# Optimization experiments

Hardware: AMD Instinct MI355X
Metric: run time of the kernel (lower is better)

The kernel has to match this reference:

```python
import jax, jax.numpy as jnp
import numpy as np

B, S, HQ, HKV, D = 2, 1024, 32, 8, 128

def setup_inputs() -> dict:
    key = jax.random.key(0)
    k1, k2, k3 = jax.random.split(key, 3)
    xq = jax.random.normal(k1, (B, S, HQ, D), dtype=jnp.float32)
    xk = jax.random.normal(k2, (B, S, HKV, D), dtype=jnp.float32)
    xv = jax.random.normal(k3, (B, S, HKV, D), dtype=jnp.float32)
    kv_buffer = jnp.zeros((B * S, 2 * HKV, D), dtype=jnp.float32)
    cur_select_index = jnp.arange(B * S, dtype=jnp.int64 if jax.config.read('jax_enable_x64') else jnp.int32)
    return {"xq": xq, "xk": xk, "xv": xv, "kv_buffer": kv_buffer,
            "cur_select_index": cur_select_index}


def reference(xq, xk, xv, kv_buffer, cur_select_index):
    b, s, hq, d = xq.shape
    hkv = xk.shape[2]
    group = hq // hkv

    # --- KV-cache scatter write: kv_buffer[cur_select_index] = cat(k, v) ---
    combined_kv = jnp.concatenate([xk, xv], axis=2).reshape(-1, 2 * hkv, d)
    kv_buffer_new = kv_buffer.at[cur_select_index].set(combined_kv)

    # --- causal flash-style prefill attention (GQA: repeat kv heads) ---
    scale = 1.0 / np.sqrt(d).astype(np.float32)
    k = jnp.repeat(xk, group, axis=2)  # [b, s, hq, d]
    v = jnp.repeat(xv, group, axis=2)

    scores = jnp.einsum('bqhd,bkhd->bhqk', xq, k) * scale  # [b, hq, s, s]
    causal = jnp.tril(jnp.ones((s, s), dtype=bool))
    scores = jnp.where(causal[None, None], scores, jnp.finfo(scores.dtype).min)
    attn = jax.nn.softmax(scores, axis=-1)
    out = jnp.einsum('bhqk,bkhd->bqhd', attn, v)  # [b, s, hq, d]
    out = out.reshape(b, s, hq * d)
    return out, kv_buffer_new
```

## Files before the change

kernel.cpp:

```cpp
#include <hip/hip_runtime.h>
#include <math.h>

#define B_  2
#define S_  1024
#define HQ_ 32
#define HKV_ 8
#define D_  128

typedef __bf16 bf16x8 __attribute__((ext_vector_type(8)));
typedef float  floatx4 __attribute__((ext_vector_type(4)));

static __device__ __forceinline__ unsigned pack2(float hi, float lo) {
    return __builtin_amdgcn_perm(__float_as_uint(hi), __float_as_uint(lo), 0x07060302u);
}

__global__ void kv_scatter_kernel(const float* __restrict__ xk,
                                  const float* __restrict__ xv,
                                  const int* __restrict__ sel,
                                  float* __restrict__ kv_out) {
    const int total = B_ * S_ * 2 * HKV_ * D_ / 4;
    for (int g = blockIdx.x * 256 + threadIdx.x; g < total; g += gridDim.x * 256) {
        const int t      = g >> 9;
        const int within = g & 511;
        const int idx    = sel[t];
        const float4* src = (within < 256)
            ? ((const float4*)(xk + (size_t)t * (HKV_ * D_)) + within)
            : ((const float4*)(xv + (size_t)t * (HKV_ * D_)) + (within - 256));
        ((float4*)(kv_out + (size_t)idx * (2 * HKV_ * D_)))[within] = *src;
    }
}

__global__ __launch_bounds__(256, 2)
void attn_kernel(const float* __restrict__ xq, const float* __restrict__ xk,
                 const float* __restrict__ xv, float* __restrict__ out) {
    const int lid = blockIdx.x;
    const int hk  = lid & 7;
    const int j   = lid >> 3;
    const int qq  = j & 31;
    const int b   = j >> 5;
    const int qt  = b ? (31 - qq) : qq;

    const int tid  = threadIdx.x;
    const int wave = tid >> 6;
    const int lane = tid & 63;
    const int l15  = lane & 15;
    const int quad = lane >> 4;
    const int L    = lane & 31;
    const int hi32 = lane >> 5;
    const int h    = hk * 4 + wave;

    __shared__ __align__(16) unsigned short Kl[2][32][136];
    __shared__ __align__(16) unsigned int   Vp[2][128][16];

    bf16x8 qf[2][4];
#pragma unroll
    for (int mt = 0; mt < 2; ++mt) {
        const int row = qt * 32 + mt * 16 + l15;
        const float* qp = xq + (((size_t)(b * S_ + row)) * HQ_ + h) * D_ + quad * 8;
#pragma unroll
        for (int ks = 0; ks < 4; ++ks) {
            union { bf16x8 v; unsigned u[4]; } t2;
            const float4 f0 = *(const float4*)(qp + ks * 32);
            const float4 f1 = *(const float4*)(qp + ks * 32 + 4);
            t2.u[0] = pack2(f0.y, f0.x); t2.u[1] = pack2(f0.w, f0.z);
            t2.u[2] = pack2(f1.y, f1.x); t2.u[3] = pack2(f1.w, f1.z);
            qf[mt][ks] = t2.v;
        }
    }

    bf16x8 ones;
    { union { bf16x8 v; unsigned u[4]; } o;
      o.u[0] = o.u[1] = o.u[2] = o.u[3] = 0x3F803F80u; ones = o.v; }

    floatx4 acc[2][8];
    floatx4 lacc[2];
#pragma unroll
    for (int mt = 0; mt < 2; ++mt) {
        lacc[mt] = (floatx4){0.f, 0.f, 0.f, 0.f};
#pragma unroll
        for (int n = 0; n < 8; ++n) acc[mt][n] = (floatx4){0.f, 0.f, 0.f, 0.f};
    }

    const float scale2 = 0.12751741f;

    float4 pk[4], pv[4];
    const int keyw = wave * 2 + hi32;

    auto loads = [&](int t) {
        const size_t base = ((size_t)(b * S_ + t * 32 + keyw) * HKV_ + hk) * D_ + 4 * L;
#pragma unroll
        for (int i = 0; i < 4; ++i) {
            pk[i] = *(const float4*)(xk + base + (size_t)i * 8 * HKV_ * D_);
            pv[i] = *(const float4*)(xv + base + (size_t)i * 8 * HKV_ * D_);
        }
    };

    auto writesLDS = [&](int bi) {
#pragma unroll
        for (int i = 0; i < 4; ++i) {
            const int key = i * 8 + keyw;
            unsigned kw0 = pack2(pk[i].y, pk[i].x), kw1 = pack2(pk[i].w, pk[i].z);
            *(uint2*)&Kl[bi][key][4 * L] = make_uint2(kw0, kw1);
            unsigned D10 = pack2(pv[i].y, pv[i].x), D32 = pack2(pv[i].w, pv[i].z);
            unsigned P10 = (unsigned)__shfl_xor((int)D10, 32);
            unsigned P32 = (unsigned)__shfl_xor((int)D32, 32);
            unsigned w0 = hi32 ? __builtin_amdgcn_perm(D10, P10, 0x07060302u)
                               : __builtin_amdgcn_perm(P10, D10, 0x05040100u);
            unsigned w2 = hi32 ? __builtin_amdgcn_perm(D32, P32, 0x07060302u)
                               : __builtin_amdgcn_perm(P32, D32, 0x05040100u);
            const int col = 4 * ((i + L) & 3) + wave;
            Vp[bi][4 * L + hi32][col]     = w0;
            Vp[bi][4 * L + hi32 + 2][col] = w2;
        }
    };

    auto compute = [&](int bi, bool lastTile) {
#pragma unroll
        for (int mt = 0; mt < 2; ++mt) {
            floatx4 s0 = (floatx4){0.f, 0.f, 0.f, 0.f};
            floatx4 s1 = (floatx4){0.f, 0.f, 0.f, 0.f};
            const bool skipHi = lastTile && (mt == 0);
#pragma unroll
            for (int ks = 0; ks < 4; ++ks) {
                bf16x8 kb0 = *(const bf16x8*)&Kl[bi][l15][ks * 32 + quad * 8];
                s0 = __builtin_amdgcn_mfma_f32_16x16x32_bf16(kb0, qf[mt][ks], s0, 0, 0, 0);
                if (!skipHi) {
                    bf16x8 kb1 = *(const bf16x8*)&Kl[bi][16 + l15][ks * 32 + quad * 8];
                    s1 = __builtin_amdgcn_mfma_f32_16x16x32_bf16(kb1, qf[mt][ks], s1, 0, 0, 0);
                }
            }
            float p0[4], p1[4];
            if (lastTile) {
                const int mq = mt * 16 + l15;
#pragma unroll
                for (int r = 0; r < 4; ++r) {
                    const int k0 = quad * 4 + r;
                    p0[r] = (k0 <= mq) ? __builtin_amdgcn_exp2f(s0[r] * scale2) : 0.f;
                    p1[r] = (!skipHi && k0 + 16 <= mq)
                            ? __builtin_amdgcn_exp2f(s1[r] * scale2) : 0.f;
                }
            } else {
#pragma unroll
                for (int r = 0; r < 4; ++r) {
                    p0[r] = __builtin_amdgcn_exp2f(s0[r] * scale2);
                    p1[r] = __builtin_amdgcn_exp2f(s1[r] * scale2);
                }
            }
            unsigned a0 = pack2(p0[1], p0[0]);
            unsigned a1 = pack2(p0[3], p0[2]);
            unsigned b0 = pack2(p1[1], p1[0]);
            unsigned b1 = pack2(p1[3], p1[2]);
            const int addr0 = (l15 + 16 * ((2 * quad)     & 3)) << 2;
            const int addr1 = (l15 + 16 * ((2 * quad + 1) & 3)) << 2;
            union { bf16x8 v; unsigned u[4]; } pau;
            {
                unsigned ta = (unsigned)__builtin_amdgcn_ds_bpermute(addr0, (int)a0);
                unsigned tb = (unsigned)__builtin_amdgcn_ds_bpermute(addr0, (int)b0);
                pau.u[0] = (quad < 2) ? ta : tb;
            }
            {
                unsigned ta = (unsigned)__builtin_amdgcn_ds_bpermute(addr0, (int)a1);
                unsigned tb = (unsigned)__builtin_amdgcn_ds_bpermute(addr0, (int)b1);
                pau.u[1] = (quad < 2) ? ta : tb;
            }
            {
                unsigned ta = (unsigned)__builtin_amdgcn_ds_bpermute(addr1, (int)a0);
                unsigned tb = (unsigned)__builtin_amdgcn_ds_bpermute(addr1, (int)b0);
                pau.u[2] = (quad < 2) ? ta : tb;
            }
            {
                unsigned ta = (unsigned)__builtin_amdgcn_ds_bpermute(addr1, (int)a1);
                unsigned tb = (unsigned)__builtin_amdgcn_ds_bpermute(addr1, (int)b1);
                pau.u[3] = (quad < 2) ? ta : tb;
            }
            bf16x8 pa = pau.v;
            lacc[mt] = __builtin_amdgcn_mfma_f32_16x16x32_bf16(pa, ones, lacc[mt], 0, 0, 0);
#pragma unroll
            for (int n = 0; n < 8; ++n) {
                const int d  = n * 16 + l15;
                const int cb = 4 * ((quad + (d >> 2)) & 3);
                bf16x8 vb = *(const bf16x8*)&Vp[bi][d][cb];
                acc[mt][n] = __builtin_amdgcn_mfma_f32_16x16x32_bf16(pa, vb, acc[mt][n], 0, 0, 0);
            }
        }
    };

    const int nkt = qt + 1;
    loads(0);
    writesLDS(0);
    __syncthreads();
    for (int t = 0; t + 1 < nkt; ++t) {
        const int bi = t & 1;
        loads(t + 1);
        compute(bi, false);
        writesLDS(1 - bi);
        __syncthreads();
    }
    compute((nkt - 1) & 1, true);

#pragma unroll
    for (int mt = 0; mt < 2; ++mt) {
#pragma unroll
        for (int r = 0; r < 4; ++r) {
            const float inv = __builtin_amdgcn_rcpf(lacc[mt][r]);
            const int row = qt * 32 + mt * 16 + quad * 4 + r;
            float* op = out + (((size_t)(b * S_ + row)) * HQ_ + h) * D_ + l15;
#pragma unroll
            for (int n = 0; n < 8; ++n) op[n * 16] = acc[mt][n][r] * inv;
        }
    }
}

extern "C" void kernel_launch(void* const* d_in, const int* in_sizes, int n_in,
                              void* d_out, int out_size, void* d_ws, size_t ws_size,
                              hipStream_t stream) {
    const float* xq  = (const float*)d_in[0];
    const float* xk  = (const float*)d_in[1];
    const float* xv  = (const float*)d_in[2];
    const int*   sel = (const int*)d_in[4];

    float* out    = (float*)d_out;
    float* kv_out = out + (size_t)B_ * S_ * HQ_ * D_;

    kv_scatter_kernel<<<dim3(512), dim3(256), 0, stream>>>(xk, xv, sel, kv_out);
    attn_kernel<<<dim3(512), dim3(256), 0, stream>>>(xq, xk, xv, out);
}
```

Measured before the change: 152.1 us.

## Split causal key tiles across two wave groups per block with LDS reduction

Doubles the block to 512 threads. The two 4-wave halves each handle about half of the causal key tiles for the same query tile and heads, using separate double-buffered K/V LDS regions. At the end, half 1 writes its partial output accumulators and row sums into reused LDS, and half 0 adds them, normalises and stores. This shortens the serial key loop per block and adds waves per CU. The cost is extra LDS, a combine step, and launch bounds of (512,4), which may force a tight register budget and cause spills.

Measured after the change: 371.4 us. +144.2%, slower.

```diff
diff --git a/kernel.cpp b/kernel.cpp
--- a/kernel.cpp
+++ b/kernel.cpp
@@ -30,7 +30,7 @@
     }
 }
 
-__global__ __launch_bounds__(256, 2)
+__global__ __launch_bounds__(512, 4)
 void attn_kernel(const float* __restrict__ xq, const float* __restrict__ xk,
                  const float* __restrict__ xv, float* __restrict__ out) {
     const int lid = blockIdx.x;
@@ -42,15 +42,21 @@
 
     const int tid  = threadIdx.x;
     const int wave = tid >> 6;
+    const int hw   = wave & 3;
+    const int half = wave >> 2;
     const int lane = tid & 63;
     const int l15  = lane & 15;
     const int quad = lane >> 4;
     const int L    = lane & 31;
     const int hi32 = lane >> 5;
-    const int h    = hk * 4 + wave;
-
-    __shared__ __align__(16) unsigned short Kl[2][32][136];
-    __shared__ __align__(16) unsigned int   Vp[2][128][16];
+    const int h    = hk * 4 + hw;
+
+    __shared__ __align__(16) unsigned short Kl[2][2][32][136];
+    __shared__ __align__(16) unsigned int   Vp[2][2][128][16];
+    __shared__ __align__(16) float          Lx[8][256];
+
+    unsigned short (*Kh)[32][136] = Kl[half];
+    unsigned int   (*Vh)[128][16] = Vp[half];
 
     bf16x8 qf[2][4];
 #pragma unroll
@@ -84,7 +90,7 @@
     const float scale2 = 0.12751741f;
 
     float4 pk[4], pv[4];
-    const int keyw = wave * 2 + hi32;
+    const int keyw = hw * 2 + hi32;
 
     auto loads = [&](int t) {
         const size_t base = ((size_t)(b * S_ + t * 32 + keyw) * HKV_ + hk) * D_ + 4 * L;
@@ -100,7 +106,7 @@
         for (int i = 0; i < 4; ++i) {
             const int key = i * 8 + keyw;
             unsigned kw0 = pack2(pk[i].y, pk[i].x), kw1 = pack2(pk[i].w, pk[i].z);
-            *(uint2*)&Kl[bi][key][4 * L] = make_uint2(kw0, kw1);
+            *(uint2*)&Kh[bi][key][4 * L] = make_uint2(kw0, kw1);
             unsigned D10 = pack2(pv[i].y, pv[i].x), D32 = pack2(pv[i].w, pv[i].z);
             unsigned P10 = (unsigned)__shfl_xor((int)D10, 32);
             unsigned P32 = (unsigned)__shfl_xor((int)D32, 32);
@@ -108,9 +114,9 @@
                                : __builtin_amdgcn_perm(P10, D10, 0x05040100u);
             unsigned w2 = hi32 ? __builtin_amdgcn_perm(D32, P32, 0x07060302u)
                                : __builtin_amdgcn_perm(P32, D32, 0x05040100u);
-            const int col = 4 * ((i + L) & 3) + wave;
-            Vp[bi][4 * L + hi32][col]     = w0;
-            Vp[bi][4 * L + hi32 + 2][col] = w2;
+            const int col = 4 * ((i + L) & 3) + hw;
+            Vh[bi][4 * L + hi32][col]     = w0;
+            Vh[bi][4 * L + hi32 + 2][col] = w2;
         }
     };
 
@@ -122,10 +128,10 @@
             const bool skipHi = lastTile && (mt == 0);
 #pragma unroll
             for (int ks = 0; ks < 4; ++ks) {
-                bf16x8 kb0 = *(const bf16x8*)&Kl[bi][l15][ks * 32 + quad * 8];
+                bf16x8 kb0 = *(const bf16x8*)&Kh[bi][l15][ks * 32 + quad * 8];
                 s0 = __builtin_amdgcn_mfma_f32_16x16x32_bf16(kb0, qf[mt][ks], s0, 0, 0, 0);
                 if (!skipHi) {
-                    bf16x8 kb1 = *(const bf16x8*)&Kl[bi][16 + l15][ks * 32 + quad * 8];
+                    bf16x8 kb1 = *(const bf16x8*)&Kh[bi][16 + l15][ks * 32 + quad * 8];
                     s1 = __builtin_amdgcn_mfma_f32_16x16x32_bf16(kb1, qf[mt][ks], s1, 0, 0, 0);
                 }
             }
@@ -179,34 +185,74 @@
             for (int n = 0; n < 8; ++n) {
                 const int d  = n * 16 + l15;
                 const int cb = 4 * ((quad + (d >> 2)) & 3);
-                bf16x8 vb = *(const bf16x8*)&Vp[bi][d][cb];
+                bf16x8 vb = *(const bf16x8*)&Vh[bi][d][cb];
                 acc[mt][n] = __builtin_amdgcn_mfma_f32_16x16x32_bf16(pa, vb, acc[mt][n], 0, 0, 0);
             }
         }
     };
 
-    const int nkt = qt + 1;
-    loads(0);
-    writesLDS(0);
+    const int nkt   = qt + 1;
+    const int n1    = nkt >> 1;
+    const int n0    = nkt - n1;
+    const int nmine = half ? n1 : n0;
+    const int tbase = half ? 0 : n1;
+
+    if (nmine > 0) { loads(tbase); writesLDS(0); }
     __syncthreads();
-    for (int t = 0; t + 1 < nkt; ++t) {
-        const int bi = t & 1;
-        loads(t + 1);
+    for (int s = 0; s + 1 < n0; ++s) {
+        const int bi = s & 1;
+        const bool pf = (s + 1 < nmine);
+        if (pf) loads(tbase + s + 1);
         compute(bi, false);
-        writesLDS(1 - bi);
+        if (pf) writesLDS(1 - bi);
         __syncthreads();
     }
-    compute((nkt - 1) & 1, true);
-
-#pragma unroll
-    for (int mt = 0; mt < 2; ++mt) {
-#pragma unroll
-        for (int r = 0; r < 4; ++r) {
-            const float inv = __builtin_amdgcn_rcpf(lacc[mt][r]);
-            const int row = qt * 32 + mt * 16 + quad * 4 + r;
-            float* op = out + (((size_t)(b * S_ + row)) * HQ_ + h) * D_ + l15;
-#pragma unroll
-            for (int n = 0; n < 8; ++n) op[n * 16] = acc[mt][n][r] * inv;
+    if (half == 0)          compute((n0 - 1) & 1, true);
+    else if (n1 == n0)      compute((n0 - 1) & 1, false);
+    __syncthreads();
+
+    float* cbA = (float*)Kl;
+    float* cbB = (float*)Vp;
+    const int sl = hw * 64 + lane;
+    if (half == 1) {
+#pragma unroll
+        for (int n = 0; n < 8; ++n)
+#pragma unroll
+            for (int r = 0; r < 4; ++r) {
+                cbA[(n * 4 + r) * 256 + sl] = acc[0][n][r];
+                cbB[(n * 4 + r) * 256 + sl] = acc[1][n][r];
+            }
+#pragma unroll
+        for (int mt = 0; mt < 2; ++mt)
+#pragma unroll
+            for (int r = 0; r < 4; ++r)
+                Lx[mt * 4 + r][sl] = lacc[mt][r];
+    }
+    __syncthreads();
+    if (half == 0) {
+#pragma unroll
+        for (int n = 0; n < 8; ++n)
+#pragma unroll
+            for (int r = 0; r < 4; ++r) {
+                acc[0][n][r] += cbA[(n * 4 + r) * 256 + sl];
+                acc[1][n][r] += cbB[(n * 4 + r) * 256 + sl];
+            }
+#pragma unroll
+        for (int mt = 0; mt < 2; ++mt)
+#pragma unroll
+            for (int r = 0; r < 4; ++r)
+                lacc[mt][r] += Lx[mt * 4 + r][sl];
+
+#pragma unroll
+        for (int mt = 0; mt < 2; ++mt) {
+#pragma unroll
+            for (int r = 0; r < 4; ++r) {
+                const float inv = __builtin_amdgcn_rcpf(lacc[mt][r]);
+                const int row = qt * 32 + mt * 16 + quad * 4 + r;
+                float* op = out + (((size_t)(b * S_ + row)) * HQ_ + h) * D_ + l15;
+#pragma unroll
+                for (int n = 0; n < 8; ++n) op[n * 16] = acc[mt][n][r] * inv;
+            }
         }
     }
 }
@@ -223,5 +269,5 @@
     float* kv_out = out + (size_t)B_ * S_ * HQ_ * D_;
 
     kv_scatter_kernel<<<dim3(512), dim3(256), 0, stream>>>(xk, xv, sel, kv_out);
-    attn_kernel<<<dim3(512), dim3(256), 0, stream>>>(xq, xk, xv, out);
-}
+    attn_kernel<<<dim3(512), dim3(512), 0, stream>>>(xq, xk, xv, out);
+}
```
